# Performance work log

Hardware: AMD Instinct MI355X
Metric: run time of the kernel (lower is better)

## Reference

```python
import jax, jax.numpy as jnp
import numpy as np

VOCAB = 50000
D = 512


def setup_inputs() -> dict:
    key = jax.random.key(0)
    ks = jax.random.split(key, 8)
    B, LP, LH = 64, 256, 384
    inputs_pre = jax.random.randint(ks[0], (B, LP), 0, VOCAB, dtype=jnp.int32)
    inputs_hyp = jax.random.randint(ks[1], (B, LH), 0, VOCAB, dtype=jnp.int32)
    content_mask = jnp.ones((B, LP), dtype=jnp.int32)
    cit_content_mask = jnp.ones((B, LH), dtype=jnp.int32)
    emb = jax.random.normal(ks[2], (VOCAB, D), dtype=jnp.float32) * 0.1
    # classify: Linear(4d, d) -> ReLU -> Linear(d, 1) -> Sigmoid  (W stored [in, out])
    W1 = jax.random.normal(ks[3], (4 * D, D), dtype=jnp.float32) * 0.02
    b1 = jnp.zeros((D,), dtype=jnp.float32)
    W2 = jax.random.normal(ks[4], (D, 1), dtype=jnp.float32) * 0.02
    b2 = jnp.zeros((1,), dtype=jnp.float32)
    return {"inputs_pre": inputs_pre, "inputs_hyp": inputs_hyp,
            "content_mask": content_mask, "cit_content_mask": cit_content_mask,
            "emb": emb, "W1": W1, "b1": b1, "W2": W2, "b2": b2}


def reference(inputs_pre, inputs_hyp, content_mask, cit_content_mask, emb, W1, b1, W2, b2):
    # eval mode: dropout is identity; ones masks => truncation is a no-op
    pre = emb[inputs_pre]   # [B, LP, D]
    hyp = emb[inputs_hyp]   # [B, LH, D]
    # attFunction: relu(bmm) -> dual-axis softmax -> two bmms -> concat
    alphas = jax.nn.relu(jnp.einsum('bpd,bhd->bph', pre, hyp))  # [B, LP, LH]
    alphas_pre = jax.nn.softmax(alphas, axis=1)  # softmax over LP (dim=1)
    alphas_hyp = jax.nn.softmax(alphas, axis=2)  # softmax over LH (dim=2)
    pre_att = jnp.einsum('bph,bhd->bpd', alphas_pre, hyp)   # [B, LP, D]
    hyp_att = jnp.einsum('bph,bpd->bhd', alphas_hyp, pre)   # [B, LH, D]
    m_pre = jnp.concatenate([pre, pre_att], axis=2)   # [B, LP, 2D]
    m_hyp = jnp.concatenate([hyp, hyp_att], axis=2)   # [B, LH, 2D]
    pre_sum = jnp.sum(m_pre, axis=1)  # [B, 2D]
    hyp_sum = jnp.sum(m_hyp, axis=1)  # [B, 2D]
    pre_hyp = jnp.concatenate([pre_sum, hyp_sum], axis=1)  # [B, 4D]
    h = jax.nn.relu(pre_hyp @ W1 + b1)
    return jax.nn.sigmoid(h @ W2 + b2)  # [B, 1]
```

## Files before the change

### kernel.cpp

```cpp
#include <hip/hip_runtime.h>
#include <math.h>

#define B    64
#define LP   256
#define LH   384
#define D    512
#define CH   64
#define BBLK 2

__global__ __launch_bounds__(512)
void gather_sum_kernel(const int* __restrict__ idx_pre,
                       const int* __restrict__ idx_hyp,
                       const float* __restrict__ emb,
                       float* __restrict__ Sp,
                       float* __restrict__ Sh) {
    const int b = blockIdx.y;
    int c = blockIdx.x;

    const int* idx;
    float* S;
    if (c < LP / CH) {
        idx = idx_pre + b * LP;
        S = Sp;
    } else {
        idx = idx_hyp + b * LH;
        S = Sh;
        c -= LP / CH;
    }

    __shared__ int sidx[CH];
    if (threadIdx.x < CH) sidx[threadIdx.x] = idx[c * CH + threadIdx.x];
    __syncthreads();

    const int sub = threadIdx.x >> 7;
    const int c4  = threadIdx.x & 127;

    float4 acc = make_float4(0.f, 0.f, 0.f, 0.f);
#pragma unroll
    for (int rr = 0; rr < CH / 4; ++rr) {
        const int r = (rr << 2) + sub;
        const float4 v = *reinterpret_cast<const float4*>(
            emb + (size_t)sidx[r] * D + (c4 << 2));
        acc.x += v.x; acc.y += v.y; acc.z += v.z; acc.w += v.w;
    }

    __shared__ float4 red[4][128];
    red[sub][c4] = acc;
    __syncthreads();

    const int t = threadIdx.x;
    const float* rp = reinterpret_cast<const float*>(&red[0][0]);
    const float v = (rp[t] + rp[512 + t]) + (rp[1024 + t] + rp[1536 + t]);
    atomicAdd(&S[b * D + t], v);
}

__global__ __launch_bounds__(256)
void mlp1_kernel(const float* __restrict__ Sp,
                 const float* __restrict__ Sh,
                 const float* __restrict__ W1,
                 const float* __restrict__ b1,
                 float* __restrict__ H) {
    const int t  = threadIdx.x;
    const int j4 = t & 15;
    const int dq = t >> 4;
    const int j0 = blockIdx.x * 64 + j4 * 4;
    const int b0 = blockIdx.y * BBLK;

    __shared__ float sp[BBLK][D];
    __shared__ float sh[BBLK][D];
    {
        float4* spv = reinterpret_cast<float4*>(&sp[0][0]);
        float4* shv = reinterpret_cast<float4*>(&sh[0][0]);
        const float4* gp = reinterpret_cast<const float4*>(Sp + (size_t)b0 * D);
        const float4* gh = reinterpret_cast<const float4*>(Sh + (size_t)b0 * D);
        for (int i = t; i < BBLK * D / 4; i += 256) {
            spv[i] = gp[i];
            shv[i] = gh[i];
        }
    }
    __syncthreads();

    float4 acc[BBLK];
#pragma unroll
    for (int bb = 0; bb < BBLK; ++bb) acc[bb] = make_float4(0.f, 0.f, 0.f, 0.f);

    for (int i = 0; i < 32; ++i) {
        const int d = dq + (i << 4);
        const float4 wa0 = *reinterpret_cast<const float4*>(W1 + (size_t)d * D + j0);
        const float4 wa1 = *reinterpret_cast<const float4*>(W1 + (size_t)(3 * D + d) * D + j0);
        const float4 wb0 = *reinterpret_cast<const float4*>(W1 + (size_t)(D + d) * D + j0);
        const float4 wb1 = *reinterpret_cast<const float4*>(W1 + (size_t)(2 * D + d) * D + j0);
        const float4 wa = make_float4(wa0.x + wa1.x, wa0.y + wa1.y,
                                      wa0.z + wa1.z, wa0.w + wa1.w);
        const float4 wb = make_float4(wb0.x + wb1.x, wb0.y + wb1.y,
                                      wb0.z + wb1.z, wb0.w + wb1.w);
#pragma unroll
        for (int bb = 0; bb < BBLK; ++bb) {
            const float a = sp[bb][d];
            const float h = sh[bb][d];
            acc[bb].x += a * wa.x + h * wb.x;
            acc[bb].y += a * wa.y + h * wb.y;
            acc[bb].z += a * wa.z + h * wb.z;
            acc[bb].w += a * wa.w + h * wb.w;
        }
    }

    __shared__ float4 red[16][BBLK][16];
#pragma unroll
    for (int bb = 0; bb < BBLK; ++bb) red[dq][bb][j4] = acc[bb];
    __syncthreads();

    if (t < BBLK * 64) {
        const int bb = t >> 6;
        const int jj = t & 63;
        const int j  = blockIdx.x * 64 + jj;
        const float* rp = reinterpret_cast<const float*>(&red[0][0][0]);
        float s = b1[j];
#pragma unroll
        for (int q = 0; q < 16; ++q)
            s += rp[q * (BBLK * 64) + bb * 64 + jj];
        H[(size_t)(b0 + bb) * D + j] = s > 0.f ? s : 0.f;
    }
}

__global__ __launch_bounds__(256)
void mlp2_kernel(const float* __restrict__ H,
                 const float* __restrict__ W2,
                 const float* __restrict__ b2,
                 float* __restrict__ out) {
    const int b = blockIdx.x;
    const int t = threadIdx.x;

    float v = H[(size_t)b * D + t] * W2[t]
            + H[(size_t)b * D + 256 + t] * W2[256 + t];

#pragma unroll
    for (int off = 32; off > 0; off >>= 1) v += __shfl_down(v, off);

    __shared__ float part[4];
    if ((t & 63) == 0) part[t >> 6] = v;
    __syncthreads();
    if (t == 0) {
        const float s = part[0] + part[1] + part[2] + part[3] + b2[0];
        out[b] = 1.f / (1.f + expf(-s));
    }
}

extern "C" void kernel_launch(void* const* d_in, const int* in_sizes, int n_in,
                              void* d_out, int out_size, void* d_ws, size_t ws_size,
                              hipStream_t stream) {
    const int*   inputs_pre = (const int*)d_in[0];
    const int*   inputs_hyp = (const int*)d_in[1];
    const float* emb = (const float*)d_in[4];
    const float* W1  = (const float*)d_in[5];
    const float* b1  = (const float*)d_in[6];
    const float* W2  = (const float*)d_in[7];
    const float* b2  = (const float*)d_in[8];
    float* out = (float*)d_out;

    float* Sp = (float*)d_ws;
    float* Sh = Sp + B * D;
    float* H  = Sh + B * D;

    hipMemsetAsync(d_ws, 0, (size_t)2 * B * D * sizeof(float), stream);

    dim3 g1((LP + LH) / CH, B);
    gather_sum_kernel<<<g1, 512, 0, stream>>>(inputs_pre, inputs_hyp, emb, Sp, Sh);

    dim3 g2(D / 64, B / BBLK);
    mlp1_kernel<<<g2, 256, 0, stream>>>(Sp, Sh, W1, b1, H);

    mlp2_kernel<<<B, 256, 0, stream>>>(H, W2, b2, out);
}
```

Baseline: 173.7 us.

## Replace atomic accumulation with per-chunk partials reduced in MLP kernel, narrow column tiles

The gather kernel now writes per-chunk partial sums to a workspace buffer instead of using atomicAdd, which also removes the memset launch. The first MLP kernel reduces the 10 partials while loading its inputs. Its column tile is halved from 64 to 32, doubling the block count to 512. The trade-off is extra partial-buffer traffic and redundant reductions repeated across more blocks.

Result: no change. 174.0 us (+0.2%).

```diff
diff --git a/kernel.cpp b/kernel.cpp
--- a/kernel.cpp
+++ b/kernel.cpp
@@ -6,30 +6,24 @@
 #define LH   384
 #define D    512
 #define CH   64
+#define NCP  (LP / CH)
+#define NCH  (LH / CH)
+#define NC   (NCP + NCH)
 #define BBLK 2
+#define JW   32
 
 __global__ __launch_bounds__(512)
 void gather_sum_kernel(const int* __restrict__ idx_pre,
                        const int* __restrict__ idx_hyp,
                        const float* __restrict__ emb,
-                       float* __restrict__ Sp,
-                       float* __restrict__ Sh) {
+                       float* __restrict__ P) {
     const int b = blockIdx.y;
-    int c = blockIdx.x;
-
-    const int* idx;
-    float* S;
-    if (c < LP / CH) {
-        idx = idx_pre + b * LP;
-        S = Sp;
-    } else {
-        idx = idx_hyp + b * LH;
-        S = Sh;
-        c -= LP / CH;
-    }
+    const int c = blockIdx.x;
+    const int* idx = (c < NCP) ? (idx_pre + b * LP + c * CH)
+                               : (idx_hyp + b * LH + (c - NCP) * CH);
 
     __shared__ int sidx[CH];
-    if (threadIdx.x < CH) sidx[threadIdx.x] = idx[c * CH + threadIdx.x];
+    if (threadIdx.x < CH) sidx[threadIdx.x] = idx[threadIdx.x];
     __syncthreads();
 
     const int sub = threadIdx.x >> 7;
@@ -51,31 +45,41 @@
     const int t = threadIdx.x;
     const float* rp = reinterpret_cast<const float*>(&red[0][0]);
     const float v = (rp[t] + rp[512 + t]) + (rp[1024 + t] + rp[1536 + t]);
-    atomicAdd(&S[b * D + t], v);
+    P[((size_t)c * B + b) * D + t] = v;
 }
 
 __global__ __launch_bounds__(256)
-void mlp1_kernel(const float* __restrict__ Sp,
-                 const float* __restrict__ Sh,
+void mlp1_kernel(const float* __restrict__ P,
                  const float* __restrict__ W1,
                  const float* __restrict__ b1,
                  float* __restrict__ H) {
     const int t  = threadIdx.x;
-    const int j4 = t & 15;
-    const int dq = t >> 4;
-    const int j0 = blockIdx.x * 64 + j4 * 4;
+    const int j4 = t & 7;
+    const int dq = t >> 3;
+    const int j0 = blockIdx.x * JW + j4 * 4;
     const int b0 = blockIdx.y * BBLK;
 
     __shared__ float sp[BBLK][D];
     __shared__ float sh[BBLK][D];
     {
+        const float4* Pv = reinterpret_cast<const float4*>(P);
         float4* spv = reinterpret_cast<float4*>(&sp[0][0]);
         float4* shv = reinterpret_cast<float4*>(&sh[0][0]);
-        const float4* gp = reinterpret_cast<const float4*>(Sp + (size_t)b0 * D);
-        const float4* gh = reinterpret_cast<const float4*>(Sh + (size_t)b0 * D);
         for (int i = t; i < BBLK * D / 4; i += 256) {
-            spv[i] = gp[i];
-            shv[i] = gh[i];
+            float4 a = make_float4(0.f, 0.f, 0.f, 0.f);
+#pragma unroll
+            for (int c = 0; c < NCP; ++c) {
+                const float4 v = Pv[((size_t)c * B + b0) * (D / 4) + i];
+                a.x += v.x; a.y += v.y; a.z += v.z; a.w += v.w;
+            }
+            spv[i] = a;
+            float4 h = make_float4(0.f, 0.f, 0.f, 0.f);
+#pragma unroll
+            for (int c = NCP; c < NC; ++c) {
+                const float4 v = Pv[((size_t)c * B + b0) * (D / 4) + i];
+                h.x += v.x; h.y += v.y; h.z += v.z; h.w += v.w;
+            }
+            shv[i] = h;
         }
     }
     __syncthreads();
@@ -84,8 +88,8 @@
 #pragma unroll
     for (int bb = 0; bb < BBLK; ++bb) acc[bb] = make_float4(0.f, 0.f, 0.f, 0.f);
 
-    for (int i = 0; i < 32; ++i) {
-        const int d = dq + (i << 4);
+    for (int i = 0; i < D / 32; ++i) {
+        const int d = dq + (i << 5);
         const float4 wa0 = *reinterpret_cast<const float4*>(W1 + (size_t)d * D + j0);
         const float4 wa1 = *reinterpret_cast<const float4*>(W1 + (size_t)(3 * D + d) * D + j0);
         const float4 wb0 = *reinterpret_cast<const float4*>(W1 + (size_t)(D + d) * D + j0);
@@ -105,20 +109,20 @@
         }
     }
 
-    __shared__ float4 red[16][BBLK][16];
+    __shared__ float4 red[32][BBLK][8];
 #pragma unroll
     for (int bb = 0; bb < BBLK; ++bb) red[dq][bb][j4] = acc[bb];
     __syncthreads();
 
-    if (t < BBLK * 64) {
-        const int bb = t >> 6;
-        const int jj = t & 63;
-        const int j  = blockIdx.x * 64 + jj;
+    if (t < BBLK * JW) {
+        const int bb = t >> 5;
+        const int jj = t & 31;
+        const int j  = blockIdx.x * JW + jj;
         const float* rp = reinterpret_cast<const float*>(&red[0][0][0]);
         float s = b1[j];
 #pragma unroll
-        for (int q = 0; q < 16; ++q)
-            s += rp[q * (BBLK * 64) + bb * 64 + jj];
+        for (int q = 0; q < 32; ++q)
+            s += rp[(q * BBLK + bb) * JW + jj];
         H[(size_t)(b0 + bb) * D + j] = s > 0.f ? s : 0.f;
     }
 }
@@ -158,17 +162,14 @@
     const float* b2  = (const float*)d_in[8];
     float* out = (float*)d_out;
 
-    float* Sp = (float*)d_ws;
-    float* Sh = Sp + B * D;
-    float* H  = Sh + B * D;
+    float* P = (float*)d_ws;
+    float* H = P + (size_t)NC * B * D;
 
-    hipMemsetAsync(d_ws, 0, (size_t)2 * B * D * sizeof(float), stream);
+    dim3 g1(NC, B);
+    gather_sum_kernel<<<g1, 512, 0, stream>>>(inputs_pre, inputs_hyp, emb, P);
 
-    dim3 g1((LP + LH) / CH, B);
-    gather_sum_kernel<<<g1, 512, 0, stream>>>(inputs_pre, inputs_hyp, emb, Sp, Sh);
-
-    dim3 g2(D / 64, B / BBLK);
-    mlp1_kernel<<<g2, 256, 0, stream>>>(Sp, Sh, W1, b1, H);
+    dim3 g2(D / JW, B / BBLK);
+    mlp1_kernel<<<g2, 256, 0, stream>>>(P, W1, b1, H);
 
     mlp2_kernel<<<B, 256, 0, stream>>>(H, W2, b2, out);
 }
```
